# Kernel optimization log

Measured on AMD Instinct MI355X. Metric: run time of the kernel, lower is better.

Reference implementation:

```python
import jax, jax.numpy as jnp
import numpy as np

K = 5            # neighbors
TEMP = 1.0       # softmax temperature
BANK = 1000      # fixed bank capacity in source
B = 65536        # batch
D = 256          # feature_dim
EPS = 1e-12      # F.normalize eps


def _l2norm(x):
    # F.normalize(x, dim=1): x / max(||x||, eps)
    n = jnp.sqrt(jnp.sum(x * x, axis=1, keepdims=True))
    return x / jnp.maximum(n, EPS)


def setup_inputs() -> dict:
    key = jax.random.key(0)
    k1, k2, k3, k4 = jax.random.split(key, 4)
    features = jax.random.normal(k1, (B, D), dtype=jnp.float32)
    feature_bank = jax.random.normal(k2, (BANK, D), dtype=jnp.float32)
    # fusion_layer: Linear(2D -> D), ReLU, Linear(D -> D). torch weight layout [out, in].
    W1 = jax.random.normal(k3, (D, 2 * D), dtype=jnp.float32) * (1.0 / np.sqrt(2 * D))
    b1 = jnp.zeros((D,), dtype=jnp.float32)
    W2 = jax.random.normal(k4, (D, D), dtype=jnp.float32) * (1.0 / np.sqrt(D))
    b2 = jnp.zeros((D,), dtype=jnp.float32)
    return {"features": features, "feature_bank": feature_bank,
            "W1": W1, "b1": b1, "W2": W2, "b2": b2}


def reference(features, feature_bank, W1, b1, W2, b2):
    # knn_search: cosine similarity against the (full) bank
    qn = _l2norm(features)                      # [B, D]
    bn = _l2norm(feature_bank)                  # [BANK, D]
    sims = qn @ bn.T                            # [B, BANK]
    top_s, top_i = jax.lax.top_k(sims, K)       # [B, K]
    w = jax.nn.softmax(top_s / TEMP, axis=1)    # [B, K]
    neigh = feature_bank[top_i]                 # gather -> [B, K, D]
    nf = jnp.einsum('bkd,bk->bd', neigh, w)     # weighted average of neighbors
    # fusion MLP on concat([query, neighbors])
    fused = jnp.concatenate([features, nf], axis=1)    # [B, 2D]
    h = jax.nn.relu(fused @ W1.T + b1)                 # [B, D]
    out = h @ W2.T + b2                                # [B, D]
    return out
```

## Files before the change

kernel.cpp:

```cpp
#include <hip/hip_runtime.h>

#define DIM 256
#define NC 12

typedef __attribute__((ext_vector_type(8))) short short8;
typedef __attribute__((ext_vector_type(4))) float f32x4;

__device__ __forceinline__ short f32bf(float f) {
    unsigned u = __builtin_bit_cast(unsigned, f);
    unsigned r = u + 0x7FFFu + ((u >> 16) & 1u);
    return (short)(r >> 16);
}

__device__ __forceinline__ void gld_lds16(const void* g, void* l) {
    __builtin_amdgcn_global_load_lds((const __attribute__((address_space(1))) unsigned int*)g,
                                     (__attribute__((address_space(3))) unsigned int*)l, 16, 0, 0);
}

template<int CTRL>
__device__ __forceinline__ unsigned dppmax(unsigned x) {
    unsigned y = (unsigned)__builtin_amdgcn_update_dpp(0, (int)x, CTRL, 0xF, 0xF, true);
    return x > y ? x : y;
}

__global__ __launch_bounds__(256) void k_prep(const float* __restrict__ bank,
        const float* __restrict__ W1, const float* __restrict__ W2,
        short* __restrict__ bnbf, double* __restrict__ binv,
        short* __restrict__ w1bf, short* __restrict__ w2bf)
{
    __shared__ double part[4];
    __shared__ double s_inv;
    const int bid = blockIdx.x, t = threadIdx.x;
    if (bid < 1024) {
        const int row = bid;
        if (row < 1000) {
            float v = bank[(size_t)row * DIM + t];
            double ssq = (double)v * (double)v;
            for (int o = 32; o > 0; o >>= 1) ssq += __shfl_down(ssq, o);
            if ((t & 63) == 0) part[t >> 6] = ssq;
            __syncthreads();
            if (t == 0) {
                double s = part[0] + part[1] + part[2] + part[3];
                double n = sqrt(s); if (n < 1e-12) n = 1e-12;
                double inv = 1.0 / n;
                binv[row] = inv; s_inv = inv;
            }
            __syncthreads();
            const int pcol = (((t >> 3) ^ (row & 7)) << 3) | (t & 7);
            bnbf[(size_t)row * DIM + pcol] = f32bf((float)((double)v * s_inv));
        } else {
            bnbf[(size_t)row * DIM + t] = 0;
            if (t == 0) binv[row] = 0.0;
        }
    } else if (bid < 1536) {
        const int i = (bid - 1024) * 256 + t;
        w1bf[i] = f32bf(W1[i]);
    } else {
        const int i = (bid - 1536) * 256 + t;
        w2bf[i] = f32bf(W2[i]);
    }
}

__global__ __launch_bounds__(256) void k_sims(const float* __restrict__ feat,
        const short* __restrict__ bnbf, short* __restrict__ sims,
        int* __restrict__ top, int qoff)
{
    __shared__ alignas(16) short Qs[32 * 264];
    __shared__ alignas(16) short Ab[64 * 256];
    const int t = threadIdx.x, lane = t & 63, w = t >> 6;
    const int n16 = lane & 15, q4 = lane >> 4;

    {
        const int r = t >> 3, p = t & 7;
        const float4* src = (const float4*)(feat + (size_t)(qoff + blockIdx.x * 32 + r) * DIM + p * 32);
        short* dst = Qs + r * 264 + p * 32;
        #pragma unroll
        for (int i = 0; i < 8; ++i) {
            float4 v = src[i];
            dst[i*4+0] = f32bf(v.x); dst[i*4+1] = f32bf(v.y);
            dst[i*4+2] = f32bf(v.z); dst[i*4+3] = f32bf(v.w);
        }
    }
    const char* gA = (const char*)bnbf;
    char* lA = (char*)Ab;
    #pragma unroll
    for (int i = 0; i < 8; ++i)
        gld_lds16(gA + i * 4096 + t * 16, lA + i * 4096 + (t >> 6) * 1024);
    __syncthreads();

    short8 bq[8][2];
    #pragma unroll
    for (int kc = 0; kc < 8; ++kc)
        #pragma unroll
        for (int nt = 0; nt < 2; ++nt)
            bq[kc][nt] = *(const short8*)(Qs + (nt * 16 + n16) * 264 + kc * 32 + q4 * 8);

    const int ml = w * 16 + n16;
    int aoff[8];
    #pragma unroll
    for (int kc = 0; kc < 8; ++kc)
        aoff[kc] = (ml * 256 + (((kc * 4 + q4) ^ (ml & 7)) << 3)) * 2;

    const f32x4 vzero = {0.f, 0.f, 0.f, 0.f};
    for (int chunk = 0; chunk < 16; ++chunk) {
        f32x4 acc[2];
        acc[0] = vzero; acc[1] = vzero;
        #pragma unroll
        for (int kc = 0; kc < 8; ++kc) {
            short8 af = *(const short8*)(lA + aoff[kc]);
            #pragma unroll
            for (int nt = 0; nt < 2; ++nt)
                acc[nt] = __builtin_amdgcn_mfma_f32_16x16x32_bf16(af, bq[kc][nt], acc[nt], 0, 0, 0);
        }
        const int bankb = chunk * 64 + w * 16 + q4 * 4;
        #pragma unroll
        for (int nt = 0; nt < 2; ++nt) {
            const int qc = blockIdx.x * 32 + nt * 16 + n16;
            uint2 u;
            u.x = ((unsigned)(unsigned short)f32bf(acc[nt][0])) |
                  (((unsigned)(unsigned short)f32bf(acc[nt][1])) << 16);
            u.y = ((unsigned)(unsigned short)f32bf(acc[nt][2])) |
                  (((unsigned)(unsigned short)f32bf(acc[nt][3])) << 16);
            *(uint2*)(sims + (size_t)qc * 1024 + bankb) = u;
        }
        __syncthreads();
        if (chunk < 15) {
            #pragma unroll
            for (int i = 0; i < 8; ++i)
                gld_lds16(gA + (size_t)(chunk + 1) * 32768 + i * 4096 + t * 16,
                          lA + i * 4096 + (t >> 6) * 1024);
            __syncthreads();
        }
    }

    for (int i = 0; i < 8; ++i) {
        const int q = blockIdx.x * 32 + w * 8 + i;
        const uint4* p = (const uint4*)(sims + (size_t)q * 1024 + lane * 16);
        uint4 a = p[0], b = p[1];

        unsigned k[16];
        {
            unsigned words[8] = {a.x, a.y, a.z, a.w, b.x, b.y, b.z, b.w};
            #pragma unroll
            for (int j = 0; j < 16; ++j) {
                unsigned h = (j & 1) ? (words[j >> 1] >> 16) : (words[j >> 1] & 0xFFFFu);
                unsigned m = (h ^ 0x8000u) ^ ((0u - (h >> 15)) & 0x7FFFu);
                int idx = lane * 16 + j;
                k[j] = (idx < 1000) ? ((m << 16) | (unsigned)idx) : 0u;
            }
        }
        #pragma unroll
        for (int sz = 2; sz <= 16; sz <<= 1)
            #pragma unroll
            for (int st = sz >> 1; st >= 1; st >>= 1)
                #pragma unroll
                for (int ii = 0; ii < 16; ++ii) {
                    int j = ii ^ st;
                    if (j > ii) {
                        bool desc = ((ii & sz) == 0);
                        unsigned lo = k[ii], hi = k[j];
                        unsigned mx = lo > hi ? lo : hi;
                        unsigned mn = lo > hi ? hi : lo;
                        k[ii] = desc ? mx : mn;
                        k[j] = desc ? mn : mx;
                    }
                }
        unsigned mine = 0;
        #pragma unroll
        for (int r = 0; r < 12; ++r) {
            unsigned m = k[0];
            m = dppmax<0xB1>(m);
            m = dppmax<0x4E>(m);
            m = dppmax<0x141>(m);
            m = dppmax<0x140>(m);
            m = dppmax<0x142>(m);
            m = dppmax<0x143>(m);
            unsigned wm = (unsigned)__builtin_amdgcn_readlane((int)m, 63);
            if (lane == r) mine = wm;
            if (k[0] == wm) {
                #pragma unroll
                for (int s = 0; s < 12; ++s) k[s] = k[s + 1];
            }
        }
        if (lane < 12) top[(size_t)(qoff + q) * NC + lane] = (int)(mine & 0xFFFFu);
    }
}

__global__ __launch_bounds__(256) void k_refine(const float* __restrict__ feat,
        const float* __restrict__ bank, const int* __restrict__ top,
        const double* __restrict__ binv, short* __restrict__ nf,
        short* __restrict__ featbf)
{
    __shared__ int    cidxL[16 * NC];
    __shared__ float  bdF[16 * NC];
    __shared__ double bdD[16 * NC];
    __shared__ float  simsF[16 * NC];
    __shared__ double simsD[16 * NC];
    __shared__ float  qiL[16];
    __shared__ int    flagL[16];
    __shared__ int    selidx[16][5];
    __shared__ float  selw[16][5];

    const int t = threadIdx.x, lane = t & 63, w = t >> 6;
    const int g = lane >> 4, u = lane & 15;
    const int ql = w * 4 + g;
    const int qbase = blockIdx.x * 16;
    const int q = qbase + ql;

    if (t < 16 * NC) {
        const int c = top[(size_t)qbase * NC + t];
        cidxL[t] = c;
        const double b = binv[c];
        bdD[t] = b; bdF[t] = (float)b;
    }
    __syncthreads();

    int ci[NC];
    #pragma unroll
    for (int c = 0; c < NC; ++c) ci[c] = cidxL[ql * NC + c];

    float qf[16];
    float ssf = 0.f;
    #pragma unroll
    for (int j = 0; j < 4; ++j) {
        float4 v = *(const float4*)(feat + (size_t)q * DIM + j * 64 + u * 4);
        qf[j*4+0] = v.x; qf[j*4+1] = v.y; qf[j*4+2] = v.z; qf[j*4+3] = v.w;
        ssf += v.x*v.x + v.y*v.y + v.z*v.z + v.w*v.w;
    }
    {
        short* fb = featbf + (size_t)q * DIM + u * 4;
        #pragma unroll
        for (int j = 0; j < 4; ++j) {
            uint2 pk;
            pk.x = ((unsigned)(unsigned short)f32bf(qf[j*4+0])) |
                   (((unsigned)(unsigned short)f32bf(qf[j*4+1])) << 16);
            pk.y = ((unsigned)(unsigned short)f32bf(qf[j*4+2])) |
                   (((unsigned)(unsigned short)f32bf(qf[j*4+3])) << 16);
            *(uint2*)(fb + j * 64) = pk;
        }
    }
    #pragma unroll
    for (int o = 1; o < 16; o <<= 1) ssf += __shfl_xor(ssf, o, 16);
    float nq = sqrtf(ssf); if (nq < 1e-12f) nq = 1e-12f;
    if (u == 0) qiL[ql] = 1.f / nq;

    float s[NC];
    #pragma unroll
    for (int c = 0; c < NC; ++c) {
        const float* brow = bank + (size_t)ci[c] * DIM + u * 4;
        float a0 = 0.f, a1 = 0.f, a2 = 0.f, a3 = 0.f;
        #pragma unroll
        for (int j = 0; j < 4; ++j) {
            float4 b = *(const float4*)(brow + j * 64);
            a0 += qf[j*4+0] * b.x; a1 += qf[j*4+1] * b.y;
            a2 += qf[j*4+2] * b.z; a3 += qf[j*4+3] * b.w;
        }
        s[c] = (a0 + a1) + (a2 + a3);
    }
    #pragma unroll
    for (int o = 1; o < 16; o <<= 1)
        #pragma unroll
        for (int c = 0; c < NC; ++c) s[c] += __shfl_xor(s[c], o, 16);
    #pragma unroll
    for (int c = 0; c < NC; ++c) if (u == c) simsF[ql * NC + c] = s[c];
    __syncthreads();

    if (t < 16) {
        const float qi2 = qiL[t];
        float vf[NC];
        unsigned long long key[NC];
        int cid[NC];
        #pragma unroll
        for (int c = 0; c < NC; ++c) {
            cid[c] = cidxL[t * NC + c];
            float v = simsF[t * NC + c] * qi2 * bdF[t * NC + c];
            vf[c] = v;
            unsigned ub = __builtin_bit_cast(unsigned, v);
            unsigned m = (ub >> 31) ? ~ub : (ub | 0x80000000u);
            key[c] = ((unsigned long long)m << 10) | (unsigned long long)(1023 - cid[c]);
        }
        int rank[NC];
        #pragma unroll
        for (int c = 0; c < NC; ++c) rank[c] = 0;
        #pragma unroll
        for (int c1 = 0; c1 < NC; ++c1)
            #pragma unroll
            for (int c2 = c1 + 1; c2 < NC; ++c2) {
                const bool gt = key[c1] > key[c2];
                rank[c2] += gt ? 1 : 0;
                rank[c1] += gt ? 0 : 1;
            }
        float v5 = 0.f, v6 = 0.f;
        #pragma unroll
        for (int c = 0; c < NC; ++c) {
            v5 += (rank[c] == 4) ? vf[c] : 0.f;
            v6 += (rank[c] == 5) ? vf[c] : 0.f;
        }
        flagL[t] = (v5 - v6) < 2e-6f;

        float vm = vf[0];
        #pragma unroll
        for (int c = 1; c < NC; ++c) vm = fmaxf(vm, vf[c]);
        float e[NC]; float wsum = 0.f;
        #pragma unroll
        for (int c = 0; c < NC; ++c) {
            float ex = __expf(vf[c] - vm);
            ex = (rank[c] < 5) ? ex : 0.f;
            e[c] = ex; wsum += ex;
        }
        const float inv = 1.f / wsum;
        #pragma unroll
        for (int k = 0; k < 5; ++k) {
            int idx = 0; float wv = 0.f;
            #pragma unroll
            for (int c = 0; c < NC; ++c) {
                const bool is = (rank[c] == k);
                idx += is ? cid[c] : 0;
                wv  += is ? e[c]  : 0.f;
            }
            selidx[t][k] = idx; selw[t][k] = wv * inv;
        }
    }
    __syncthreads();

    if (flagL[ql]) {
        double ssd = 0.0;
        #pragma unroll
        for (int j = 0; j < 16; ++j) ssd += (double)qf[j] * (double)qf[j];
        #pragma unroll
        for (int o = 1; o < 16; o <<= 1) ssd += __shfl_xor(ssd, o, 16);
        double nd = sqrt(ssd); if (nd < 1e-12) nd = 1e-12;
        const double qid = 1.0 / nd;
        double sd[NC];
        #pragma unroll
        for (int c = 0; c < NC; ++c) {
            const float* brow = bank + (size_t)ci[c] * DIM + u * 4;
            double a0 = 0, a1 = 0, a2 = 0, a3 = 0;
            #pragma unroll
            for (int j = 0; j < 4; ++j) {
                float4 b = *(const float4*)(brow + j * 64);
                a0 += (double)qf[j*4+0] * b.x; a1 += (double)qf[j*4+1] * b.y;
                a2 += (double)qf[j*4+2] * b.z; a3 += (double)qf[j*4+3] * b.w;
            }
            sd[c] = (a0 + a1) + (a2 + a3);
        }
        #pragma unroll
        for (int o = 1; o < 16; o <<= 1)
            #pragma unroll
            for (int c = 0; c < NC; ++c) sd[c] += __shfl_xor(sd[c], o, 16);
        #pragma unroll
        for (int c = 0; c < NC; ++c)
            if (u == c) simsD[ql * NC + c] = sd[c] * qid * bdD[ql * NC + c];
    }
    __syncthreads();

    if (t < 16 && flagL[t]) {
        double vd[NC];
        unsigned long long key[NC];
        int cid[NC];
        #pragma unroll
        for (int c = 0; c < NC; ++c) {
            cid[c] = cidxL[t * NC + c];
            double v = simsD[t * NC + c];
            vd[c] = v;
            unsigned long long ub = __builtin_bit_cast(unsigned long long, v);
            unsigned long long m = (ub >> 63) ? ~ub : (ub | 0x8000000000000000ULL);
            key[c] = (m & ~0x3FFULL) | (unsigned long long)(1023 - cid[c]);
        }
        int rank[NC];
        #pragma unroll
        for (int c = 0; c < NC; ++c) rank[c] = 0;
        #pragma unroll
        for (int c1 = 0; c1 < NC; ++c1)
            #pragma unroll
            for (int c2 = c1 + 1; c2 < NC; ++c2) {
                const bool gt = key[c1] > key[c2];
                rank[c2] += gt ? 1 : 0;
                rank[c1] += gt ? 0 : 1;
            }
        float vf[NC];
        #pragma unroll
        for (int c = 0; c < NC; ++c) vf[c] = (float)vd[c];
        float vm = vf[0];
        #pragma unroll
        for (int c = 1; c < NC; ++c) vm = fmaxf(vm, vf[c]);
        float e[NC]; float wsum = 0.f;
        #pragma unroll
        for (int c = 0; c < NC; ++c) {
            float ex = __expf(vf[c] - vm);
            ex = (rank[c] < 5) ? ex : 0.f;
            e[c] = ex; wsum += ex;
        }
        const float inv = 1.f / wsum;
        #pragma unroll
        for (int k = 0; k < 5; ++k) {
            int idx = 0; float wv = 0.f;
            #pragma unroll
            for (int c = 0; c < NC; ++c) {
                const bool is = (rank[c] == k);
                idx += is ? cid[c] : 0;
                wv  += is ? e[c]  : 0.f;
            }
            selidx[t][k] = idx; selw[t][k] = wv * inv;
        }
    }
    __syncthreads();

    float wk[5]; int ik[5];
    #pragma unroll
    for (int k = 0; k < 5; ++k) { wk[k] = selw[ql][k]; ik[k] = selidx[ql][k]; }
    float4 oa[4];
    #pragma unroll
    for (int j = 0; j < 4; ++j) { oa[j].x = 0.f; oa[j].y = 0.f; oa[j].z = 0.f; oa[j].w = 0.f; }
    #pragma unroll
    for (int k = 0; k < 5; ++k) {
        const float wc = wk[k];
        const float* brow = bank + (size_t)ik[k] * DIM + u * 4;
        #pragma unroll
        for (int j = 0; j < 4; ++j) {
            float4 b = *(const float4*)(brow + j * 64);
            oa[j].x += wc * b.x; oa[j].y += wc * b.y;
            oa[j].z += wc * b.z; oa[j].w += wc * b.w;
        }
    }
    short* od = nf + (size_t)q * DIM + u * 4;
    #pragma unroll
    for (int j = 0; j < 4; ++j) {
        uint2 pk;
        pk.x = ((unsigned)(unsigned short)f32bf(oa[j].x)) |
               (((unsigned)(unsigned short)f32bf(oa[j].y)) << 16);
        pk.y = ((unsigned)(unsigned short)f32bf(oa[j].z)) |
               (((unsigned)(unsigned short)f32bf(oa[j].w)) << 16);
        *(uint2*)(od + j * 64) = pk;
    }
}

__global__ __launch_bounds__(256, 4) void k_mlp(const short* __restrict__ featbf,
        const short* __restrict__ nf, const short* __restrict__ w1bf,
        const short* __restrict__ w2bf, const float* __restrict__ b1,
        const float* __restrict__ b2, float* __restrict__ out)
{
    __shared__ alignas(16) short Hs[64 * 264];
    const int t = threadIdx.x, lane = t & 63, w = t >> 6;
    const int mb = blockIdx.x * 64;
    const int n16 = lane & 15, ko = (lane >> 4) << 3;
    const int rq = (lane >> 4) << 2, cc = lane & 15;
    const f32x4 vzero = {0.f, 0.f, 0.f, 0.f};

    f32x4 acc[4][4];
    #pragma unroll
    for (int a = 0; a < 4; ++a)
        #pragma unroll
        for (int b = 0; b < 4; ++b) acc[a][b] = vzero;

    const short* A0 = featbf + (size_t)mb * 256 + ko;
    const short* A1 = nf     + (size_t)mb * 256 + ko;
    const short* Wp = w1bf + (size_t)(w * 64 + n16) * 512 + ko;

    #pragma unroll
    for (int kc = 0; kc < 8; ++kc) {
        short8 af[4], bf[4];
        #pragma unroll
        for (int mt = 0; mt < 4; ++mt)
            af[mt] = *(const short8*)(A0 + (mt * 16 + n16) * 256 + kc * 32);
        #pragma unroll
        for (int nt = 0; nt < 4; ++nt)
            bf[nt] = *(const short8*)(Wp + (size_t)nt * 16 * 512 + kc * 32);
        #pragma unroll
        for (int mt = 0; mt < 4; ++mt)
            #pragma unroll
            for (int nt = 0; nt < 4; ++nt)
                acc[mt][nt] = __builtin_amdgcn_mfma_f32_16x16x32_bf16(af[mt], bf[nt], acc[mt][nt], 0, 0, 0);
    }
    #pragma unroll
    for (int kc = 0; kc < 8; ++kc) {
        short8 af[4], bf[4];
        #pragma unroll
        for (int mt = 0; mt < 4; ++mt)
            af[mt] = *(const short8*)(A1 + (mt * 16 + n16) * 256 + kc * 32);
        #pragma unroll
        for (int nt = 0; nt < 4; ++nt)
            bf[nt] = *(const short8*)(Wp + (size_t)nt * 16 * 512 + (kc + 8) * 32);
        #pragma unroll
        for (int mt = 0; mt < 4; ++mt)
            #pragma unroll
            for (int nt = 0; nt < 4; ++nt)
                acc[mt][nt] = __builtin_amdgcn_mfma_f32_16x16x32_bf16(af[mt], bf[nt], acc[mt][nt], 0, 0, 0);
    }

    #pragma unroll
    for (int mt = 0; mt < 4; ++mt)
        #pragma unroll
        for (int nt = 0; nt < 4; ++nt) {
            const int row = mt * 16 + rq;
            const int col = w * 64 + nt * 16 + cc;
            const float bias = b1[col];
            #pragma unroll
            for (int rr = 0; rr < 4; ++rr) {
                float v = acc[mt][nt][rr] + bias;
                Hs[(row + rr) * 264 + col] = f32bf(fmaxf(v, 0.f));
            }
        }
    #pragma unroll
    for (int a = 0; a < 4; ++a)
        #pragma unroll
        for (int b = 0; b < 4; ++b) acc[a][b] = vzero;
    __syncthreads();

    #pragma unroll
    for (int kc = 0; kc < 8; ++kc) {
        short8 bf[4];
        #pragma unroll
        for (int nt = 0; nt < 4; ++nt)
            bf[nt] = *(const short8*)(w2bf + (size_t)(w * 64 + nt * 16 + n16) * 256 + kc * 32 + ko);
        short8 af[4];
        #pragma unroll
        for (int mt = 0; mt < 4; ++mt)
            af[mt] = *(const short8*)(Hs + (mt * 16 + n16) * 264 + kc * 32 + ko);
        #pragma unroll
        for (int mt = 0; mt < 4; ++mt)
            #pragma unroll
            for (int nt = 0; nt < 4; ++nt)
                acc[mt][nt] = __builtin_amdgcn_mfma_f32_16x16x32_bf16(af[mt], bf[nt], acc[mt][nt], 0, 0, 0);
    }
    #pragma unroll
    for (int mt = 0; mt < 4; ++mt)
        #pragma unroll
        for (int nt = 0; nt < 4; ++nt) {
            const int row = mb + mt * 16 + rq;
            const int col = w * 64 + nt * 16 + cc;
            const float bias = b2[col];
            #pragma unroll
            for (int rr = 0; rr < 4; ++rr)
                out[(size_t)(row + rr) * 256 + col] = acc[mt][nt][rr] + bias;
        }
}

extern "C" void kernel_launch(void* const* d_in, const int* in_sizes, int n_in,
                              void* d_out, int out_size, void* d_ws, size_t ws_size,
                              hipStream_t stream) {
    const float* feat = (const float*)d_in[0];
    const float* bank = (const float*)d_in[1];
    const float* W1   = (const float*)d_in[2];
    const float* b1   = (const float*)d_in[3];
    const float* W2   = (const float*)d_in[4];
    const float* b2   = (const float*)d_in[5];
    float* out = (float*)d_out;

    char* ws = (char*)d_ws;
    short*  bnbf = (short*)(ws + 0);
    double* binv = (double*)(ws + 524288);
    short*  w1bf = (short*)(ws + 532480);
    short*  w2bf = (short*)(ws + 794624);
    int*    top  = (int*)(ws + 925696);
    short*  nf   = (short*)(ws + 4071424);
    short*  X    = (short*)(ws + 37625856);
    short*  featbf = X;

    k_prep<<<1792, 256, 0, stream>>>(bank, W1, W2, bnbf, binv, w1bf, w2bf);
    for (int s = 0; s < 4; ++s)
        k_sims<<<512, 256, 0, stream>>>(feat, bnbf, X, top, s * 16384);
    k_refine<<<4096, 256, 0, stream>>>(feat, bank, top, binv, nf, featbf);
    k_mlp  <<<1024, 256, 0, stream>>>(featbf, nf, w1bf, w2bf, b1, b2, out);
}
```

Before: 393.0 us.

## Keep similarity rows in LDS and stream bank fragments from global into registers

The sims kernel used to write bf16 similarity rows to a global scratch buffer and read them back for the top-candidate selection. It now keeps the 32x1024 tile in shared memory, loads query fragments straight into registers, and loads bank fragments directly from global with register double-buffering, which removes the per-chunk LDS staging and barriers. The four launches become a single 2048-block launch, and the bank swizzle in prep is dropped. The risk is lower occupancy from the roughly 66KB LDS tile and the larger register count, plus bank reads that are no longer shared across waves through LDS.

```diff
diff --git a/kernel.cpp b/kernel.cpp
--- a/kernel.cpp
+++ b/kernel.cpp
@@ -10,11 +10,6 @@
     unsigned u = __builtin_bit_cast(unsigned, f);
     unsigned r = u + 0x7FFFu + ((u >> 16) & 1u);
     return (short)(r >> 16);
-}
-
-__device__ __forceinline__ void gld_lds16(const void* g, void* l) {
-    __builtin_amdgcn_global_load_lds((const __attribute__((address_space(1))) unsigned int*)g,
-                                     (__attribute__((address_space(3))) unsigned int*)l, 16, 0, 0);
 }
 
 template<int CTRL>
@@ -46,8 +41,7 @@
                 binv[row] = inv; s_inv = inv;
             }
             __syncthreads();
-            const int pcol = (((t >> 3) ^ (row & 7)) << 3) | (t & 7);
-            bnbf[(size_t)row * DIM + pcol] = f32bf((float)((double)v * s_inv));
+            bnbf[(size_t)row * DIM + t] = f32bf((float)((double)v * s_inv));
         } else {
             bnbf[(size_t)row * DIM + t] = 0;
             if (t == 0) binv[row] = 0.0;
@@ -62,80 +56,70 @@
 }
 
 __global__ __launch_bounds__(256) void k_sims(const float* __restrict__ feat,
-        const short* __restrict__ bnbf, short* __restrict__ sims,
-        int* __restrict__ top, int qoff)
+        const short* __restrict__ bnbf, int* __restrict__ top)
 {
-    __shared__ alignas(16) short Qs[32 * 264];
-    __shared__ alignas(16) short Ab[64 * 256];
+    __shared__ alignas(16) short S[32 * 1032];
     const int t = threadIdx.x, lane = t & 63, w = t >> 6;
     const int n16 = lane & 15, q4 = lane >> 4;
-
-    {
-        const int r = t >> 3, p = t & 7;
-        const float4* src = (const float4*)(feat + (size_t)(qoff + blockIdx.x * 32 + r) * DIM + p * 32);
-        short* dst = Qs + r * 264 + p * 32;
-        #pragma unroll
-        for (int i = 0; i < 8; ++i) {
-            float4 v = src[i];
-            dst[i*4+0] = f32bf(v.x); dst[i*4+1] = f32bf(v.y);
-            dst[i*4+2] = f32bf(v.z); dst[i*4+3] = f32bf(v.w);
-        }
-    }
-    const char* gA = (const char*)bnbf;
-    char* lA = (char*)Ab;
-    #pragma unroll
-    for (int i = 0; i < 8; ++i)
-        gld_lds16(gA + i * 4096 + t * 16, lA + i * 4096 + (t >> 6) * 1024);
-    __syncthreads();
+    const int qb = blockIdx.x * 32;
 
     short8 bq[8][2];
     #pragma unroll
     for (int kc = 0; kc < 8; ++kc)
         #pragma unroll
-        for (int nt = 0; nt < 2; ++nt)
-            bq[kc][nt] = *(const short8*)(Qs + (nt * 16 + n16) * 264 + kc * 32 + q4 * 8);
-
-    const int ml = w * 16 + n16;
-    int aoff[8];
+        for (int nt = 0; nt < 2; ++nt) {
+            const float4* s = (const float4*)(feat + (size_t)(qb + nt * 16 + n16) * DIM + kc * 32 + q4 * 8);
+            float4 v0 = s[0], v1 = s[1];
+            short8 f;
+            f[0] = f32bf(v0.x); f[1] = f32bf(v0.y); f[2] = f32bf(v0.z); f[3] = f32bf(v0.w);
+            f[4] = f32bf(v1.x); f[5] = f32bf(v1.y); f[6] = f32bf(v1.z); f[7] = f32bf(v1.w);
+            bq[kc][nt] = f;
+        }
+
+    const char* Abase = (const char*)bnbf + ((size_t)(w * 16 + n16) * DIM + q4 * 8) * 2;
+    const f32x4 vzero = {0.f, 0.f, 0.f, 0.f};
+
+    short8 af[8], nx[8];
     #pragma unroll
     for (int kc = 0; kc < 8; ++kc)
-        aoff[kc] = (ml * 256 + (((kc * 4 + q4) ^ (ml & 7)) << 3)) * 2;
-
-    const f32x4 vzero = {0.f, 0.f, 0.f, 0.f};
+        af[kc] = *(const short8*)(Abase + kc * 64);
+
+    #pragma unroll 2
     for (int chunk = 0; chunk < 16; ++chunk) {
-        f32x4 acc[2];
-        acc[0] = vzero; acc[1] = vzero;
+        if (chunk < 15) {
+            const char* nb = Abase + (size_t)(chunk + 1) * 32768;
+            #pragma unroll
+            for (int kc = 0; kc < 8; ++kc)
+                nx[kc] = *(const short8*)(nb + kc * 64);
+        }
+        f32x4 acc0 = vzero, acc1 = vzero;
         #pragma unroll
         for (int kc = 0; kc < 8; ++kc) {
-            short8 af = *(const short8*)(lA + aoff[kc]);
-            #pragma unroll
-            for (int nt = 0; nt < 2; ++nt)
-                acc[nt] = __builtin_amdgcn_mfma_f32_16x16x32_bf16(af, bq[kc][nt], acc[nt], 0, 0, 0);
+            acc0 = __builtin_amdgcn_mfma_f32_16x16x32_bf16(af[kc], bq[kc][0], acc0, 0, 0, 0);
+            acc1 = __builtin_amdgcn_mfma_f32_16x16x32_bf16(af[kc], bq[kc][1], acc1, 0, 0, 0);
         }
         const int bankb = chunk * 64 + w * 16 + q4 * 4;
-        #pragma unroll
-        for (int nt = 0; nt < 2; ++nt) {
-            const int qc = blockIdx.x * 32 + nt * 16 + n16;
+        {
             uint2 u;
-            u.x = ((unsigned)(unsigned short)f32bf(acc[nt][0])) |
-                  (((unsigned)(unsigned short)f32bf(acc[nt][1])) << 16);
-            u.y = ((unsigned)(unsigned short)f32bf(acc[nt][2])) |
-                  (((unsigned)(unsigned short)f32bf(acc[nt][3])) << 16);
-            *(uint2*)(sims + (size_t)qc * 1024 + bankb) = u;
-        }
-        __syncthreads();
-        if (chunk < 15) {
-            #pragma unroll
-            for (int i = 0; i < 8; ++i)
-                gld_lds16(gA + (size_t)(chunk + 1) * 32768 + i * 4096 + t * 16,
-                          lA + i * 4096 + (t >> 6) * 1024);
-            __syncthreads();
-        }
-    }
+            u.x = ((unsigned)(unsigned short)f32bf(acc0[0])) |
+                  (((unsigned)(unsigned short)f32bf(acc0[1])) << 16);
+            u.y = ((unsigned)(unsigned short)f32bf(acc0[2])) |
+                  (((unsigned)(unsigned short)f32bf(acc0[3])) << 16);
+            *(uint2*)(S + (size_t)n16 * 1032 + bankb) = u;
+            u.x = ((unsigned)(unsigned short)f32bf(acc1[0])) |
+                  (((unsigned)(unsigned short)f32bf(acc1[1])) << 16);
+            u.y = ((unsigned)(unsigned short)f32bf(acc1[2])) |
+                  (((unsigned)(unsigned short)f32bf(acc1[3])) << 16);
+            *(uint2*)(S + (size_t)(16 + n16) * 1032 + bankb) = u;
+        }
+        #pragma unroll
+        for (int kc = 0; kc < 8; ++kc) af[kc] = nx[kc];
+    }
+    __syncthreads();
 
     for (int i = 0; i < 8; ++i) {
-        const int q = blockIdx.x * 32 + w * 8 + i;
-        const uint4* p = (const uint4*)(sims + (size_t)q * 1024 + lane * 16);
+        const int ql = w * 8 + i;
+        const uint4* p = (const uint4*)(S + (size_t)ql * 1032 + lane * 16);
         uint4 a = p[0], b = p[1];
 
         unsigned k[16];
@@ -182,7 +166,7 @@
                 for (int s = 0; s < 12; ++s) k[s] = k[s + 1];
             }
         }
-        if (lane < 12) top[(size_t)(qoff + q) * NC + lane] = (int)(mine & 0xFFFFu);
+        if (lane < 12) top[(size_t)(qb + ql) * NC + lane] = (int)(mine & 0xFFFFu);
     }
 }
 
@@ -554,12 +538,10 @@
     short*  w2bf = (short*)(ws + 794624);
     int*    top  = (int*)(ws + 925696);
     short*  nf   = (short*)(ws + 4071424);
-    short*  X    = (short*)(ws + 37625856);
-    short*  featbf = X;
+    short*  featbf = (short*)(ws + 37625856);
 
     k_prep<<<1792, 256, 0, stream>>>(bank, W1, W2, bnbf, binv, w1bf, w2bf);
-    for (int s = 0; s < 4; ++s)
-        k_sims<<<512, 256, 0, stream>>>(feat, bnbf, X, top, s * 16384);
+    k_sims<<<2048, 256, 0, stream>>>(feat, bnbf, top);
     k_refine<<<4096, 256, 0, stream>>>(feat, bank, top, binv, nf, featbf);
     k_mlp  <<<1024, 256, 0, stream>>>(featbf, nf, w1bf, w2bf, b1, b2, out);
 }
```

Result: slower. 406.4 us (+3.4%).
